# Kernel optimization log

Measured on AMD Instinct MI355X. Metric: run time of the kernel, lower is better.

The kernel has to match this reference:

```python
import jax, jax.numpy as jnp
import numpy as np

N_NODES = 100000
HIDDEN = 128
N_EDGES = 640000


def setup_inputs() -> dict:
    key = jax.random.key(0)
    ks = jax.random.split(key, 9)
    X = jax.random.normal(ks[0], (N_NODES, HIDDEN), dtype=jnp.float32)
    edge_index = jax.random.randint(ks[1], (2, N_EDGES), 0, N_NODES, dtype=jnp.int64)
    s = 1.0 / np.sqrt(HIDDEN)
    W_in = jax.random.uniform(ks[2], (HIDDEN, HIDDEN), jnp.float32, -s, s)
    b_in = jax.random.uniform(ks[3], (HIDDEN,), jnp.float32, -s, s)
    W_gate = jax.random.uniform(ks[4], (HIDDEN, HIDDEN), jnp.float32, -s, s)
    b_gate = jax.random.uniform(ks[5], (HIDDEN,), jnp.float32, -s, s)
    W_out = jax.random.uniform(ks[6], (HIDDEN, HIDDEN), jnp.float32, -s, s)
    b_out = jax.random.uniform(ks[7], (HIDDEN,), jnp.float32, -s, s)
    return {"X": X, "edge_index": edge_index, "W_in": W_in, "b_in": b_in,
            "W_gate": W_gate, "b_gate": b_gate, "W_out": W_out, "b_out": b_out}


def reference(X, edge_index, W_in, b_in, W_gate, b_gate, W_out, b_out):
    src = edge_index[0]
    dst = edge_index[1]
    n = X.shape[0]
    # gather messages from source nodes, scatter-add into destinations
    messages = X[src]  # [E, d]
    agg = jax.ops.segment_sum(messages, dst, num_segments=n)  # [N, d]
    deg = jax.ops.segment_sum(jnp.ones_like(dst, dtype=X.dtype), dst, num_segments=n)
    deg = jnp.clip(deg, 1.0, None)[:, None]  # [N, 1]
    agg = agg / deg
    # gated MLP (torch Linear: x @ W.T + b)
    h = agg @ W_in.T + b_in
    g = jax.nn.sigmoid(agg @ W_gate.T + b_gate)
    out = (jax.nn.relu(h) * g) @ W_out.T + b_out
    return out
```

## Files before the change

### kernel.cpp

```cpp
#include <hip/hip_runtime.h>
#include <hip/hip_bf16.h>

#define HID 128
#define CAP 32

typedef __attribute__((ext_vector_type(8))) __bf16 bf16x8;
typedef __attribute__((ext_vector_type(4))) float f32x4;
typedef __attribute__((ext_vector_type(8))) unsigned short us8;

__device__ __forceinline__ unsigned short f2bf(float f){
  unsigned int u = __float_as_uint(f);
  unsigned int r = (u + 0x7FFFu + ((u >> 16) & 1u)) >> 16;
  return (unsigned short)r;
}

__global__ void prep_kernel(const float* __restrict__ X, uint2* __restrict__ Xb, int n4,
                            int* __restrict__ cnt, int N, int nConvBlk,
                            const float* __restrict__ Win, const float* __restrict__ Wg,
                            const float* __restrict__ Wo, unsigned short* __restrict__ wfrag){
  if ((int)blockIdx.x >= nConvBlk){
    int f = (blockIdx.x - nConvBlk)*256 + threadIdx.x;
    if (f >= 3*2048) return;
    int m = f >> 11, fi = f & 2047;
    int l = fi & 63, nfks = fi >> 6, ks = nfks & 3, nf = nfks >> 2;
    const float* W = (m == 0) ? Win : ((m == 1) ? Wg : Wo);
    int row = nf*16 + (l & 15), k0 = ks*32 + ((l >> 4) << 3);
    float4 a = *(const float4*)(W + row*HID + k0);
    float4 b = *(const float4*)(W + row*HID + k0 + 4);
    us8 o = { f2bf(a.x), f2bf(a.y), f2bf(a.z), f2bf(a.w),
              f2bf(b.x), f2bf(b.y), f2bf(b.z), f2bf(b.w) };
    *(us8*)(wfrag + (size_t)f*8) = o;
    return;
  }
  int i = blockIdx.x*256 + threadIdx.x;
  if (i < n4){
    float4 v = ((const float4*)X)[i];
    uint2 o;
    o.x = (unsigned)f2bf(v.x) | ((unsigned)f2bf(v.y) << 16);
    o.y = (unsigned)f2bf(v.z) | ((unsigned)f2bf(v.w) << 16);
    Xb[i] = o;
  }
  if (i < 32){ uint2 z; z.x = 0u; z.y = 0u; Xb[n4 + i] = z; }
  if (i < N) cnt[i] = 0;
}

__global__ void fill_kernel(const int* __restrict__ ei, int* __restrict__ cnt,
                            int* __restrict__ ell, int E){
  int e = blockIdx.x*256 + threadIdx.x;
  if (e >= E) return;
  int s = ei[e], d = ei[E + e];
  int slot = atomicAdd(&cnt[d], 1);
  if (slot < CAP) ell[((size_t)d << 5) + slot] = s;
}

__global__ __launch_bounds__(256) void gather_kernel(const unsigned int* __restrict__ Xu,
                              const int* __restrict__ ell, const int* __restrict__ cnt,
                              unsigned int* __restrict__ agg, int N){
  int wv = threadIdx.x >> 6, lane = threadIdx.x & 63;
  int n = blockIdx.x*4 + wv;
  if (n >= N) return;
  int d = cnt[n];
  float ax = 0.f, ay = 0.f;
  if (d > 0){
    int dd = (d < CAP) ? d : CAP;
    int m = dd - 1;
    int le = lane & 31; if (le > m) le = m;
    int sp = ell[((size_t)n << 5) + le];
    for (int j = 0; j < dd; j += 8){
      unsigned int p0, p1, p2, p3, p4, p5, p6, p7;
      {
        int s0 = (j+0 <= m) ? __shfl(sp, j+0) : N;
        int s1 = (j+1 <= m) ? __shfl(sp, j+1) : N;
        int s2 = (j+2 <= m) ? __shfl(sp, j+2) : N;
        int s3 = (j+3 <= m) ? __shfl(sp, j+3) : N;
        int s4 = (j+4 <= m) ? __shfl(sp, j+4) : N;
        int s5 = (j+5 <= m) ? __shfl(sp, j+5) : N;
        int s6 = (j+6 <= m) ? __shfl(sp, j+6) : N;
        int s7 = (j+7 <= m) ? __shfl(sp, j+7) : N;
        p0 = Xu[(unsigned)s0*64u + lane];
        p1 = Xu[(unsigned)s1*64u + lane];
        p2 = Xu[(unsigned)s2*64u + lane];
        p3 = Xu[(unsigned)s3*64u + lane];
        p4 = Xu[(unsigned)s4*64u + lane];
        p5 = Xu[(unsigned)s5*64u + lane];
        p6 = Xu[(unsigned)s6*64u + lane];
        p7 = Xu[(unsigned)s7*64u + lane];
      }
      ax += __uint_as_float(p0 << 16) + __uint_as_float(p1 << 16)
          + __uint_as_float(p2 << 16) + __uint_as_float(p3 << 16)
          + __uint_as_float(p4 << 16) + __uint_as_float(p5 << 16)
          + __uint_as_float(p6 << 16) + __uint_as_float(p7 << 16);
      ay += __uint_as_float(p0 & 0xFFFF0000u) + __uint_as_float(p1 & 0xFFFF0000u)
          + __uint_as_float(p2 & 0xFFFF0000u) + __uint_as_float(p3 & 0xFFFF0000u)
          + __uint_as_float(p4 & 0xFFFF0000u) + __uint_as_float(p5 & 0xFFFF0000u)
          + __uint_as_float(p6 & 0xFFFF0000u) + __uint_as_float(p7 & 0xFFFF0000u);
    }
  }
  float inv = (d > 0) ? 1.f/(float)d : 0.f;
  agg[(unsigned)n*64u + lane] = (unsigned)f2bf(ax*inv) | ((unsigned)f2bf(ay*inv) << 16);
}

__global__ __launch_bounds__(512, 4) void mlp_kernel(const unsigned short* __restrict__ aggb,
    const unsigned short* __restrict__ wfrag,
    const float* __restrict__ bin, const float* __restrict__ bg, const float* __restrict__ bo,
    float* __restrict__ out, int N){
  __shared__ unsigned short s_w[2*16384];
  __shared__ float s_bias[3*HID];
  const int tid = threadIdx.x;
  const int n0 = blockIdx.x * 128;

  for (int i = tid; i < 4096; i += 512)
    ((us8*)s_w)[i] = ((const us8*)wfrag)[i];
  if (tid < 3*HID){
    const float* bsrc = (tid < HID) ? bin : ((tid < 2*HID) ? bg : bo);
    s_bias[tid] = bsrc[tid & (HID-1)];
  }
  __syncthreads();

  const int l  = tid & 63;
  const int wv = tid >> 6;
  const int r0 = wv * 16;
  const int kq = (l >> 4) * 8;

  int arow = n0 + r0 + (l & 15); if (arow > N-1) arow = N-1;
  bf16x8 afr[4];
  #pragma unroll
  for (int ks = 0; ks < 4; ++ks)
    afr[ks] = *(const bf16x8*)(aggb + (size_t)arow*HID + ks*32 + kq);

  f32x4 acch[8], accg[8];
  #pragma unroll
  for (int nf = 0; nf < 8; ++nf){ acch[nf] = {0.f,0.f,0.f,0.f}; accg[nf] = {0.f,0.f,0.f,0.f}; }

  #pragma unroll
  for (int nf = 0; nf < 8; ++nf){
    #pragma unroll
    for (int ks = 0; ks < 4; ++ks){
      const int fb = ((nf*4 + ks)*64 + l) * 8;
      bf16x8 b1 = *(const bf16x8*)(s_w + fb);
      bf16x8 b2 = *(const bf16x8*)(s_w + 16384 + fb);
      acch[nf] = __builtin_amdgcn_mfma_f32_16x16x32_bf16(afr[ks], b1, acch[nf], 0, 0, 0);
      accg[nf] = __builtin_amdgcn_mfma_f32_16x16x32_bf16(afr[ks], b2, accg[nf], 0, 0, 0);
    }
  }

  __syncthreads();

  unsigned short* tw = s_w + 16384 + wv*2048;
  const int rrb = (l >> 4) * 4;
  #pragma unroll
  for (int nf = 0; nf < 8; ++nf){
    const int c = nf*16 + (l & 15);
    const int ks2 = c >> 5, sub = (c >> 3) & 3, e = c & 7;
    const float bi = s_bias[c], bgv = s_bias[HID + c];
    #pragma unroll
    for (int rg = 0; rg < 4; ++rg){
      float hh = acch[nf][rg] + bi;
      float gg = accg[nf][rg] + bgv;
      float t = fmaxf(hh, 0.f) * (1.f / (1.f + __expf(-gg)));
      int blk = sub*16 + rrb + rg;
      blk ^= (blk >> 4) & 3;
      tw[ks2*512 + blk*8 + e] = f2bf(t);
    }
  }

  bf16x8 tfr[4];
  #pragma unroll
  for (int ks = 0; ks < 4; ++ks)
    tfr[ks] = *(const bf16x8*)(tw + ks*512 + (size_t)(l ^ ((l >> 4) & 3))*8);

  f32x4 acco[8];
  #pragma unroll
  for (int nf = 0; nf < 8; ++nf) acco[nf] = {0.f,0.f,0.f,0.f};
  #pragma unroll
  for (int nf = 0; nf < 8; ++nf){
    #pragma unroll
    for (int ks = 0; ks < 4; ++ks){
      const int fb = ((nf*4 + ks)*64 + l) * 8;
      bf16x8 b3 = *(const bf16x8*)(wfrag + 32768 + fb);
      acco[nf] = __builtin_amdgcn_mfma_f32_16x16x32_bf16(tfr[ks], b3, acco[nf], 0, 0, 0);
    }
  }
  #pragma unroll
  for (int nf = 0; nf < 8; ++nf){
    const int c = nf*16 + (l & 15);
    const float bov = s_bias[2*HID + c];
    #pragma unroll
    for (int rg = 0; rg < 4; ++rg){
      int node = n0 + r0 + rrb + rg;
      if (node < N) out[(size_t)node*HID + c] = acco[nf][rg] + bov;
    }
  }
}

extern "C" void kernel_launch(void* const* d_in, const int* in_sizes, int n_in,
                              void* d_out, int out_size, void* d_ws, size_t ws_size,
                              hipStream_t stream){
  const float* X   = (const float*)d_in[0];
  const int*   ei  = (const int*)d_in[1];
  const float* Win = (const float*)d_in[2];
  const float* bin = (const float*)d_in[3];
  const float* Wg  = (const float*)d_in[4];
  const float* bg  = (const float*)d_in[5];
  const float* Wo  = (const float*)d_in[6];
  const float* bo  = (const float*)d_in[7];
  float* out = (float*)d_out;
  const int N = in_sizes[0] / HID;
  const int E = in_sizes[1] / 2;

  unsigned short* Xb    = (unsigned short*)d_ws;
  unsigned short* agg   = Xb + (size_t)(N+1)*HID;
  unsigned short* wfrag = agg + (size_t)N*HID;
  int* cnt = (int*)(wfrag + 3*16384);
  int* ell = cnt + N;

  const int n4 = N*HID/4;
  const int nConvBlk = (n4 + 255)/256;
  prep_kernel  <<<nConvBlk + 24, 256, 0, stream>>>(X, (uint2*)Xb, n4, cnt, N, nConvBlk,
                                                   Win, Wg, Wo, wfrag);
  fill_kernel  <<<(E + 255)/256, 256, 0, stream>>>(ei, cnt, ell, E);
  gather_kernel<<<(N + 3)/4, 256, 0, stream>>>((const unsigned int*)Xb, ell, cnt,
                                               (unsigned int*)agg, N);
  mlp_kernel   <<<(N + 127)/128, 512, 0, stream>>>(agg, wfrag, bin, bg, bo, out, N);
}
```

Baseline: 109.9 us.

## Fuse fill into prep kernel, pad counters, gather two nodes per wave

Merges the ELL fill pass and the X/weight bf16 conversion into one launch, and zeroes the degree counters with a memset instead. The counters are padded to a 64-byte stride so atomics on different nodes do not contend on the same cache line. The gather kernel now gives each half-wave one node, with lanes loading 8-byte uint2 chunks, which halves the lanes per node and doubles nodes per block. Costs include a 16x larger counter array to memset, and half-waves padding out to the larger degree of the pair.

```diff
diff --git a/kernel.cpp b/kernel.cpp
--- a/kernel.cpp
+++ b/kernel.cpp
@@ -3,6 +3,7 @@
 
 #define HID 128
 #define CAP 32
+#define CSTRIDE 16
 
 typedef __attribute__((ext_vector_type(8))) __bf16 bf16x8;
 typedef __attribute__((ext_vector_type(4))) float f32x4;
@@ -14,25 +15,38 @@
   return (unsigned short)r;
 }
 
-__global__ void prep_kernel(const float* __restrict__ X, uint2* __restrict__ Xb, int n4,
-                            int* __restrict__ cnt, int N, int nConvBlk,
+__global__ void mega_kernel(const float* __restrict__ X, uint2* __restrict__ Xb, int n4,
+                            const int* __restrict__ ei, int* __restrict__ cntp,
+                            int* __restrict__ ell, int E, int nFillBlk,
                             const float* __restrict__ Win, const float* __restrict__ Wg,
-                            const float* __restrict__ Wo, unsigned short* __restrict__ wfrag){
-  if ((int)blockIdx.x >= nConvBlk){
-    int f = (blockIdx.x - nConvBlk)*256 + threadIdx.x;
+                            const float* __restrict__ Wo, unsigned short* __restrict__ wfrag,
+                            int N){
+  int b = blockIdx.x;
+  if (b < nFillBlk){
+    int e = b*256 + threadIdx.x;
+    if (e >= E) return;
+    int s = ei[e], d = ei[E + e];
+    int slot = atomicAdd(&cntp[d*CSTRIDE], 1);
+    if (slot < CAP) ell[((size_t)d << 5) + slot] = s;
+    return;
+  }
+  b -= nFillBlk;
+  if (b < 24){
+    int f = b*256 + threadIdx.x;
     if (f >= 3*2048) return;
     int m = f >> 11, fi = f & 2047;
     int l = fi & 63, nfks = fi >> 6, ks = nfks & 3, nf = nfks >> 2;
     const float* W = (m == 0) ? Win : ((m == 1) ? Wg : Wo);
     int row = nf*16 + (l & 15), k0 = ks*32 + ((l >> 4) << 3);
     float4 a = *(const float4*)(W + row*HID + k0);
-    float4 b = *(const float4*)(W + row*HID + k0 + 4);
+    float4 bb = *(const float4*)(W + row*HID + k0 + 4);
     us8 o = { f2bf(a.x), f2bf(a.y), f2bf(a.z), f2bf(a.w),
-              f2bf(b.x), f2bf(b.y), f2bf(b.z), f2bf(b.w) };
+              f2bf(bb.x), f2bf(bb.y), f2bf(bb.z), f2bf(bb.w) };
     *(us8*)(wfrag + (size_t)f*8) = o;
     return;
   }
-  int i = blockIdx.x*256 + threadIdx.x;
+  b -= 24;
+  int i = b*256 + threadIdx.x;
   if (i < n4){
     float4 v = ((const float4*)X)[i];
     uint2 o;
@@ -41,63 +55,50 @@
     Xb[i] = o;
   }
   if (i < 32){ uint2 z; z.x = 0u; z.y = 0u; Xb[n4 + i] = z; }
-  if (i < N) cnt[i] = 0;
-}
-
-__global__ void fill_kernel(const int* __restrict__ ei, int* __restrict__ cnt,
-                            int* __restrict__ ell, int E){
-  int e = blockIdx.x*256 + threadIdx.x;
-  if (e >= E) return;
-  int s = ei[e], d = ei[E + e];
-  int slot = atomicAdd(&cnt[d], 1);
-  if (slot < CAP) ell[((size_t)d << 5) + slot] = s;
-}
-
-__global__ __launch_bounds__(256) void gather_kernel(const unsigned int* __restrict__ Xu,
-                              const int* __restrict__ ell, const int* __restrict__ cnt,
-                              unsigned int* __restrict__ agg, int N){
+}
+
+__global__ __launch_bounds__(256) void gather_kernel(const uint2* __restrict__ Xu2,
+                              const int* __restrict__ ell, const int* __restrict__ cntp,
+                              uint2* __restrict__ agg2, int N){
   int wv = threadIdx.x >> 6, lane = threadIdx.x & 63;
-  int n = blockIdx.x*4 + wv;
-  if (n >= N) return;
-  int d = cnt[n];
-  float ax = 0.f, ay = 0.f;
-  if (d > 0){
-    int dd = (d < CAP) ? d : CAP;
-    int m = dd - 1;
-    int le = lane & 31; if (le > m) le = m;
-    int sp = ell[((size_t)n << 5) + le];
-    for (int j = 0; j < dd; j += 8){
-      unsigned int p0, p1, p2, p3, p4, p5, p6, p7;
-      {
-        int s0 = (j+0 <= m) ? __shfl(sp, j+0) : N;
-        int s1 = (j+1 <= m) ? __shfl(sp, j+1) : N;
-        int s2 = (j+2 <= m) ? __shfl(sp, j+2) : N;
-        int s3 = (j+3 <= m) ? __shfl(sp, j+3) : N;
-        int s4 = (j+4 <= m) ? __shfl(sp, j+4) : N;
-        int s5 = (j+5 <= m) ? __shfl(sp, j+5) : N;
-        int s6 = (j+6 <= m) ? __shfl(sp, j+6) : N;
-        int s7 = (j+7 <= m) ? __shfl(sp, j+7) : N;
-        p0 = Xu[(unsigned)s0*64u + lane];
-        p1 = Xu[(unsigned)s1*64u + lane];
-        p2 = Xu[(unsigned)s2*64u + lane];
-        p3 = Xu[(unsigned)s3*64u + lane];
-        p4 = Xu[(unsigned)s4*64u + lane];
-        p5 = Xu[(unsigned)s5*64u + lane];
-        p6 = Xu[(unsigned)s6*64u + lane];
-        p7 = Xu[(unsigned)s7*64u + lane];
-      }
-      ax += __uint_as_float(p0 << 16) + __uint_as_float(p1 << 16)
-          + __uint_as_float(p2 << 16) + __uint_as_float(p3 << 16)
-          + __uint_as_float(p4 << 16) + __uint_as_float(p5 << 16)
-          + __uint_as_float(p6 << 16) + __uint_as_float(p7 << 16);
-      ay += __uint_as_float(p0 & 0xFFFF0000u) + __uint_as_float(p1 & 0xFFFF0000u)
-          + __uint_as_float(p2 & 0xFFFF0000u) + __uint_as_float(p3 & 0xFFFF0000u)
-          + __uint_as_float(p4 & 0xFFFF0000u) + __uint_as_float(p5 & 0xFFFF0000u)
-          + __uint_as_float(p6 & 0xFFFF0000u) + __uint_as_float(p7 & 0xFFFF0000u);
-    }
-  }
-  float inv = (d > 0) ? 1.f/(float)d : 0.f;
-  agg[(unsigned)n*64u + lane] = (unsigned)f2bf(ax*inv) | ((unsigned)f2bf(ay*inv) << 16);
+  int h = lane >> 5, cl = lane & 31;
+  int n = blockIdx.x*8 + wv*2 + h;
+  bool valid = (n < N);
+  int nn = valid ? n : N-1;
+  int d = cntp[nn*CSTRIDE];
+  int dd = (d < CAP) ? d : CAP;
+  int m = dd - 1;
+  int mc = (m < 0) ? 0 : m;
+  int le = (cl < mc) ? cl : mc;
+  int sp = (dd > 0) ? ell[((size_t)nn << 5) + le] : N;
+  int ddo = __shfl_xor(dd, 32);
+  int dmax = (dd > ddo) ? dd : ddo;
+  float a0 = 0.f, a1 = 0.f, a2 = 0.f, a3 = 0.f;
+  for (int j = 0; j < dmax; j += 4){
+    uint2 p[4];
+    #pragma unroll
+    for (int u = 0; u < 4; ++u){
+      int jj = j + u;
+      int js = (jj < mc) ? jj : mc;
+      int s = __shfl(sp, (h << 5) + js);
+      s = (jj <= m) ? s : N;
+      p[u] = Xu2[(unsigned)s*32u + cl];
+    }
+    #pragma unroll
+    for (int u = 0; u < 4; ++u){
+      a0 += __uint_as_float(p[u].x << 16);
+      a1 += __uint_as_float(p[u].x & 0xFFFF0000u);
+      a2 += __uint_as_float(p[u].y << 16);
+      a3 += __uint_as_float(p[u].y & 0xFFFF0000u);
+    }
+  }
+  if (valid){
+    float inv = (d > 0) ? 1.f/(float)d : 0.f;
+    uint2 o;
+    o.x = (unsigned)f2bf(a0*inv) | ((unsigned)f2bf(a1*inv) << 16);
+    o.y = (unsigned)f2bf(a2*inv) | ((unsigned)f2bf(a3*inv) << 16);
+    agg2[(unsigned)n*32u + cl] = o;
+  }
 }
 
 __global__ __launch_bounds__(512, 4) void mlp_kernel(const unsigned short* __restrict__ aggb,
@@ -211,15 +212,17 @@
   unsigned short* Xb    = (unsigned short*)d_ws;
   unsigned short* agg   = Xb + (size_t)(N+1)*HID;
   unsigned short* wfrag = agg + (size_t)N*HID;
-  int* cnt = (int*)(wfrag + 3*16384);
-  int* ell = cnt + N;
+  int* cntp = (int*)(wfrag + 3*16384);
+  int* ell  = cntp + (size_t)N*CSTRIDE;
 
   const int n4 = N*HID/4;
+  const int nFillBlk = (E + 255)/256;
   const int nConvBlk = (n4 + 255)/256;
-  prep_kernel  <<<nConvBlk + 24, 256, 0, stream>>>(X, (uint2*)Xb, n4, cnt, N, nConvBlk,
-                                                   Win, Wg, Wo, wfrag);
-  fill_kernel  <<<(E + 255)/256, 256, 0, stream>>>(ei, cnt, ell, E);
-  gather_kernel<<<(N + 3)/4, 256, 0, stream>>>((const unsigned int*)Xb, ell, cnt,
-                                               (unsigned int*)agg, N);
+  hipMemsetAsync(cntp, 0, (size_t)N*CSTRIDE*sizeof(int), stream);
+  mega_kernel  <<<nFillBlk + 24 + nConvBlk, 256, 0, stream>>>(X, (uint2*)Xb, n4, ei, cntp,
+                                                              ell, E, nFillBlk,
+                                                              Win, Wg, Wo, wfrag, N);
+  gather_kernel<<<(N + 7)/8, 256, 0, stream>>>((const uint2*)Xb, ell, cntp,
+                                               (uint2*)agg, N);
   mlp_kernel   <<<(N + 127)/128, 512, 0, stream>>>(agg, wfrag, bin, bg, bo, out, N);
 }
```

Measured after the change: 108.6 us. No clear change (-1.2%).
